# Kernel optimization log

Hardware: AMD Instinct MI355X
Metric: run time of the kernel (lower is better)

## Reference

```python
import jax, jax.numpy as jnp
import numpy as np

EPS = 1e-8  # torch F.cosine_similarity clamps norms at eps=1e-8


def setup_inputs() -> dict:
    key = jax.random.key(0)
    N, M, D = 1024, 20, 768  # speakers, utterances/speaker, embed dim
    embeddings = jax.random.normal(key, (N, M, D), dtype=jnp.float32)
    w = jnp.asarray(10.0, dtype=jnp.float32)  # init_w
    b = jnp.asarray(-5.0, dtype=jnp.float32)  # init_b
    return {"embeddings": embeddings, "w": w, "b": b}


def reference(embeddings, w, b):
    N, M, D = embeddings.shape
    centroids = embeddings.mean(axis=1)  # [N, D]
    # cosine similarity as one fused GEMM on normalized vectors
    e = embeddings / jnp.maximum(
        jnp.linalg.norm(embeddings, axis=-1, keepdims=True), EPS)
    c = centroids / jnp.maximum(
        jnp.linalg.norm(centroids, axis=-1, keepdims=True), EPS)
    # sim[j, i, m] = cos(e[i, m], centroid[j])  -- matches the torch loop/stack
    sim = jnp.einsum('imd,jd->jim', e, c)
    logits = w * sim + b  # [N_j, N_i, M]
    # torch: view(N*N, M).transpose(0,1).reshape(-1, N)
    #   => row index r = m*N + j, column i
    logits = jnp.transpose(logits, (2, 0, 1)).reshape(N * M, N)
    # torch labels: arange(N) expanded over M -> labels[r] = r // M
    labels = jnp.repeat(jnp.arange(N), M)
    logp = jax.nn.log_softmax(logits, axis=-1)
    loss = -jnp.mean(logp[jnp.arange(N * M), labels])
    return loss
```

## Files before the change

kernel.cpp:

```cpp
#include <hip/hip_runtime.h>
#include <hip/hip_bf16.h>
#include <cstdint>

#define N_SPK 1024
#define M_UTT 20
#define D_DIM 768
#define NM_ROWS (N_SPK * M_UTT)

static constexpr float EPS = 1e-8f;

#define WAIT_VM0   0x0F70
#define WAIT_LGKM0 0xC07F

typedef __attribute__((ext_vector_type(4))) float floatx4;

__device__ __forceinline__ void load16_to_lds(const void* g, void* l) {
    __builtin_amdgcn_global_load_lds(
        (const __attribute__((address_space(1))) uint32_t*)g,
        (__attribute__((address_space(3))) uint32_t*)l, 16, 0, 0);
}

__device__ __forceinline__ float wave_sum(float v) {
    #pragma unroll
    for (int o = 32; o > 0; o >>= 1) v += __shfl_xor(v, o);
    return v;
}

__device__ __forceinline__ unsigned short fp8pk(float a, float b) {
    return (unsigned short)(__builtin_amdgcn_cvt_pk_fp8_f32(a, b, 0, false) & 0xFFFF);
}

__global__ __launch_bounds__(384) void prep_kernel(const float* __restrict__ emb,
                                                   unsigned char* __restrict__ ehat,
                                                   unsigned char* __restrict__ chat,
                                                   int* __restrict__ ctr,
                                                   float* __restrict__ accum) {
    const int i = blockIdx.x;
    const int t = threadIdx.x;
    const int wave = t >> 6, lane = t & 63;

    if (i == 0 && t == 0) { *ctr = 0; *accum = 0.f; }

    const float2* src = (const float2*)(emb + (size_t)i * M_UTT * D_DIM);

    float2 v[M_UTT];
    float ss[M_UTT];
    float2 cen = {0.f, 0.f};
    #pragma unroll
    for (int m = 0; m < M_UTT; ++m) {
        const float2 x = src[m * 384 + t];
        v[m] = x;
        ss[m] = x.x * x.x + x.y * x.y;
        cen.x += x.x; cen.y += x.y;
    }
    cen.x *= (1.f / M_UTT); cen.y *= (1.f / M_UTT);
    float css = cen.x * cen.x + cen.y * cen.y;

    __shared__ float red[M_UTT + 1][6];
    #pragma unroll
    for (int m = 0; m < M_UTT; ++m) {
        const float s = wave_sum(ss[m]);
        if (lane == 0) red[m][wave] = s;
    }
    {
        const float s = wave_sum(css);
        if (lane == 0) red[M_UTT][wave] = s;
    }
    __syncthreads();

    #pragma unroll
    for (int m = 0; m < M_UTT; ++m) {
        const float tot = red[m][0] + red[m][1] + red[m][2] +
                          red[m][3] + red[m][4] + red[m][5];
        const float rn = 1.0f / fmaxf(sqrtf(tot), EPS);
        ((unsigned short*)(ehat + ((size_t)(m * N_SPK + i)) * D_DIM))[t] =
            fp8pk(v[m].x * rn, v[m].y * rn);
    }
    {
        const float tot = red[M_UTT][0] + red[M_UTT][1] + red[M_UTT][2] +
                          red[M_UTT][3] + red[M_UTT][4] + red[M_UTT][5];
        const float rn = 1.0f / fmaxf(sqrtf(tot), EPS);
        ((unsigned short*)(chat + (size_t)i * D_DIM))[t] =
            fp8pk(cen.x * rn, cen.y * rn);
    }
}

__global__ __launch_bounds__(64) void gemm_fused_kernel(
        const unsigned char* __restrict__ ehat,
        const unsigned char* __restrict__ chat,
        const float* __restrict__ wp,
        float* __restrict__ Psum,
        float* __restrict__ T) {
    __shared__ unsigned char As[64 * 128];
    __shared__ unsigned char Bs[64 * 128];

    const int lane = threadIdx.x;
    const int c = lane & 15;
    const int quad = lane >> 4;

    const int xcd = blockIdx.x & 7;
    const int idx = blockIdx.x >> 3;
    const int bu  = xcd * 40 + (idx >> 4);
    const int bj  = idx & 15;
    const int m   = bu >> 4;
    const int rb  = bu & 15;
    const int u0  = bu * 64;
    const int j0  = bj * 64;

    const unsigned char* Ag = ehat + (size_t)u0 * D_DIM;
    const unsigned char* Bg = chat + (size_t)j0 * D_DIM;

    int goff[8];
    #pragma unroll
    for (int s = 0; s < 8; ++s) {
        const int ci  = s * 64 + lane;
        const int row = ci >> 3;
        const int q   = (ci & 7) ^ (row & 7);
        goff[s] = row * D_DIM + q * 16;
    }

    int slotA[4][4], slotB[4][4];
    #pragma unroll
    for (int ks = 0; ks < 4; ++ks) {
        const int q = ks * 2 + (quad >> 1);
        #pragma unroll
        for (int f = 0; f < 4; ++f) {
            const int r = f * 16 + c;
            slotA[ks][f] = (r * 8 + (q ^ (r & 7))) * 16 + (quad & 1) * 8;
            slotB[ks][f] = slotA[ks][f];
        }
    }

    floatx4 acc[4][4] = {};

    #pragma unroll
    for (int s = 0; s < 8; ++s) {
        load16_to_lds(Ag + goff[s], As + (s * 64 + lane) * 16);
        load16_to_lds(Bg + goff[s], Bs + (s * 64 + lane) * 16);
    }

    for (int kt = 0; kt < 6; ++kt) {
        __builtin_amdgcn_s_waitcnt(WAIT_VM0);

        #pragma unroll
        for (int ks = 0; ks < 4; ++ks) {
            long af[4], bf[4];
            #pragma unroll
            for (int it = 0; it < 4; ++it)
                af[it] = *(const long*)(As + slotA[ks][it]);
            #pragma unroll
            for (int jt = 0; jt < 4; ++jt)
                bf[jt] = *(const long*)(Bs + slotB[ks][jt]);

            #pragma unroll
            for (int it = 0; it < 4; ++it)
                #pragma unroll
                for (int jt = 0; jt < 4; ++jt)
                    acc[it][jt] = __builtin_amdgcn_mfma_f32_16x16x32_fp8_fp8(
                        af[it], bf[jt], acc[it][jt], 0, 0, 0);
        }

        if (kt < 5) {
            const int k0 = (kt + 1) * 128;
            __builtin_amdgcn_s_waitcnt(WAIT_LGKM0);
            #pragma unroll
            for (int s = 0; s < 8; ++s) {
                load16_to_lds(Ag + goff[s] + k0, As + (s * 64 + lane) * 16);
                load16_to_lds(Bg + goff[s] + k0, Bs + (s * 64 + lane) * 16);
            }
        }
    }

    const float w = wp[0];

    #pragma unroll
    for (int jt = 0; jt < 4; ++jt) {
        float sm = 0.f;
        #pragma unroll
        for (int it = 0; it < 4; ++it)
            #pragma unroll
            for (int r = 0; r < 4; ++r)
                sm += __expf(w * (acc[it][jt][r] - 1.0f));
        sm += __shfl_xor(sm, 16);
        sm += __shfl_xor(sm, 32);
        if (quad == 0) Psum[(size_t)bu * N_SPK + j0 + jt * 16 + c] = sm;
    }

    #pragma unroll
    for (int it = 0; it < 4; ++it) {
        #pragma unroll
        for (int jt = 0; jt < 4; ++jt) {
            const int col = j0 + jt * 16 + c;
            const int g = m * N_SPK + col;
            const int istar = g / M_UTT;
            const int rloc = rb * 64 + it * 16 + quad * 4;
            #pragma unroll
            for (int r = 0; r < 4; ++r) {
                if (rloc + r == istar) T[g] = acc[it][jt][r];
            }
        }
    }
}

__global__ void combine_kernel(const float* __restrict__ Psum,
                               const float* __restrict__ T,
                               const float* __restrict__ wp,
                               int* __restrict__ ctr,
                               float* __restrict__ accum,
                               float* __restrict__ out) {
    const int p = blockIdx.x * 256 + threadIdx.x;
    const int m = p >> 10;
    const int j = p & 1023;
    const float w = wp[0];

    float S = 0.f;
    #pragma unroll
    for (int rb = 0; rb < 16; ++rb)
        S += Psum[(size_t)(m * 16 + rb) * N_SPK + j];
    const float term = w * (T[p] - 1.0f) - __logf(S);

    __shared__ float red[256];
    red[threadIdx.x] = term;
    __syncthreads();
    for (int o = 128; o > 0; o >>= 1) {
        if (threadIdx.x < o) red[threadIdx.x] += red[threadIdx.x + o];
        __syncthreads();
    }
    if (threadIdx.x == 0) {
        atomicAdd(accum, red[0]);
        __threadfence();
        const int old = atomicAdd(ctr, 1);
        if (old == 79) {
            const float a = atomicAdd(accum, 0.0f);
            out[0] = -a / (float)NM_ROWS;
        }
    }
}

extern "C" void kernel_launch(void* const* d_in, const int* in_sizes, int n_in,
                              void* d_out, int out_size, void* d_ws, size_t ws_size,
                              hipStream_t stream) {
    const float* emb = (const float*)d_in[0];
    const float* wp  = (const float*)d_in[1];
    float* out = (float*)d_out;

    char* ws = (char*)d_ws;
    unsigned char* ehat = (unsigned char*)(ws);
    unsigned char* chat = (unsigned char*)(ws + 15728640);
    float* Psum  = (float*)(ws + 16515072);
    float* T     = (float*)(ws + 17825792);
    int*   ctr   = (int*)  (ws + 17907712);
    float* accum = (float*)(ws + 17907716);

    prep_kernel<<<dim3(N_SPK), dim3(384), 0, stream>>>(emb, ehat, chat, ctr, accum);
    gemm_fused_kernel<<<dim3(5120), dim3(64), 0, stream>>>(ehat, chat, wp, Psum, T);
    combine_kernel<<<dim3(80), dim3(256), 0, stream>>>(Psum, T, wp, ctr, accum, out);
}
```

Before: 139.4 us.

## Use 128x128 four-wave GEMM tiles with double-buffered LDS K-slices

Replaces the single-wave 64x64 GEMM block with a 256-thread block computing a 128x128 tile, where each wave owns one 64x64 quadrant. Operand tiles loaded into LDS are shared across waves. The K loop now uses 64-byte slices with a double-buffered LDS ping-pong: the next slice is prefetched while the current one is consumed, and iterations are separated by __syncthreads. This is meant to cut global/L2 traffic through more tile reuse and to overlap loads with MFMA work, at the cost of block-wide barriers and lower block count (1280 blocks).

```diff
diff --git a/kernel.cpp b/kernel.cpp
--- a/kernel.cpp
+++ b/kernel.cpp
@@ -8,9 +8,6 @@
 #define NM_ROWS (N_SPK * M_UTT)
 
 static constexpr float EPS = 1e-8f;
-
-#define WAIT_VM0   0x0F70
-#define WAIT_LGKM0 0xC07F
 
 typedef __attribute__((ext_vector_type(4))) float floatx4;
 
@@ -85,72 +82,91 @@
     }
 }
 
-__global__ __launch_bounds__(64) void gemm_fused_kernel(
+__global__ __launch_bounds__(256, 5) void gemm_fused_kernel(
         const unsigned char* __restrict__ ehat,
         const unsigned char* __restrict__ chat,
         const float* __restrict__ wp,
         float* __restrict__ Psum,
         float* __restrict__ T) {
-    __shared__ unsigned char As[64 * 128];
-    __shared__ unsigned char Bs[64 * 128];
-
-    const int lane = threadIdx.x;
-    const int c = lane & 15;
+    __shared__ unsigned char As[2][128 * 64];
+    __shared__ unsigned char Bs[2][128 * 64];
+
+    const int t    = threadIdx.x;
+    const int lane = t & 63;
+    const int wid  = t >> 6;
+    const int c    = lane & 15;
     const int quad = lane >> 4;
+    const int wr   = wid >> 1;
+    const int wc   = wid & 1;
 
     const int xcd = blockIdx.x & 7;
     const int idx = blockIdx.x >> 3;
-    const int bu  = xcd * 40 + (idx >> 4);
-    const int bj  = idx & 15;
-    const int m   = bu >> 4;
-    const int rb  = bu & 15;
-    const int u0  = bu * 64;
-    const int j0  = bj * 64;
+    const int bu  = xcd * 20 + (idx >> 3);
+    const int bj  = idx & 7;
+    const int m   = bu >> 3;
+    const int rb8 = bu & 7;
+    const int u0  = bu * 128;
+    const int j0  = bj * 128;
 
     const unsigned char* Ag = ehat + (size_t)u0 * D_DIM;
     const unsigned char* Bg = chat + (size_t)j0 * D_DIM;
 
-    int goff[8];
-    #pragma unroll
-    for (int s = 0; s < 8; ++s) {
-        const int ci  = s * 64 + lane;
-        const int row = ci >> 3;
-        const int q   = (ci & 7) ^ (row & 7);
-        goff[s] = row * D_DIM + q * 16;
-    }
-
-    int slotA[4][4], slotB[4][4];
-    #pragma unroll
-    for (int ks = 0; ks < 4; ++ks) {
+    int goff[2];
+    #pragma unroll
+    for (int s = 0; s < 2; ++s) {
+        const int ci  = s * 256 + wid * 64 + lane;
+        const int row = ci >> 2;
+        const int qg  = (ci & 3) ^ ((row >> 1) & 3);
+        goff[s] = row * D_DIM + qg * 16;
+    }
+
+    int slotA[2][4], slotB[2][4];
+    #pragma unroll
+    for (int ks = 0; ks < 2; ++ks) {
         const int q = ks * 2 + (quad >> 1);
         #pragma unroll
         for (int f = 0; f < 4; ++f) {
-            const int r = f * 16 + c;
-            slotA[ks][f] = (r * 8 + (q ^ (r & 7))) * 16 + (quad & 1) * 8;
-            slotB[ks][f] = slotA[ks][f];
+            const int rA = wr * 64 + f * 16 + c;
+            const int rB = wc * 64 + f * 16 + c;
+            slotA[ks][f] = rA * 64 + ((q ^ ((rA >> 1) & 3)) * 16) + (quad & 1) * 8;
+            slotB[ks][f] = rB * 64 + ((q ^ ((rB >> 1) & 3)) * 16) + (quad & 1) * 8;
         }
     }
 
     floatx4 acc[4][4] = {};
 
     #pragma unroll
-    for (int s = 0; s < 8; ++s) {
-        load16_to_lds(Ag + goff[s], As + (s * 64 + lane) * 16);
-        load16_to_lds(Bg + goff[s], Bs + (s * 64 + lane) * 16);
-    }
-
-    for (int kt = 0; kt < 6; ++kt) {
-        __builtin_amdgcn_s_waitcnt(WAIT_VM0);
-
-        #pragma unroll
-        for (int ks = 0; ks < 4; ++ks) {
+    for (int s = 0; s < 2; ++s) {
+        load16_to_lds(Ag + goff[s], &As[0][(s * 256 + wid * 64 + lane) * 16]);
+        load16_to_lds(Bg + goff[s], &Bs[0][(s * 256 + wid * 64 + lane) * 16]);
+    }
+    __syncthreads();
+
+    #pragma unroll
+    for (int kt = 0; kt < 12; ++kt) {
+        const int cur = kt & 1;
+        const int nxt = cur ^ 1;
+
+        if (kt < 11) {
+            const int k0 = (kt + 1) * 64;
+            #pragma unroll
+            for (int s = 0; s < 2; ++s) {
+                load16_to_lds(Ag + goff[s] + k0,
+                              &As[nxt][(s * 256 + wid * 64 + lane) * 16]);
+                load16_to_lds(Bg + goff[s] + k0,
+                              &Bs[nxt][(s * 256 + wid * 64 + lane) * 16]);
+            }
+        }
+
+        #pragma unroll
+        for (int ks = 0; ks < 2; ++ks) {
             long af[4], bf[4];
             #pragma unroll
-            for (int it = 0; it < 4; ++it)
-                af[it] = *(const long*)(As + slotA[ks][it]);
-            #pragma unroll
-            for (int jt = 0; jt < 4; ++jt)
-                bf[jt] = *(const long*)(Bs + slotB[ks][jt]);
+            for (int f = 0; f < 4; ++f)
+                af[f] = *(const long*)(&As[cur][slotA[ks][f]]);
+            #pragma unroll
+            for (int f = 0; f < 4; ++f)
+                bf[f] = *(const long*)(&Bs[cur][slotB[ks][f]]);
 
             #pragma unroll
             for (int it = 0; it < 4; ++it)
@@ -160,18 +176,11 @@
                         af[it], bf[jt], acc[it][jt], 0, 0, 0);
         }
 
-        if (kt < 5) {
-            const int k0 = (kt + 1) * 128;
-            __builtin_amdgcn_s_waitcnt(WAIT_LGKM0);
-            #pragma unroll
-            for (int s = 0; s < 8; ++s) {
-                load16_to_lds(Ag + goff[s] + k0, As + (s * 64 + lane) * 16);
-                load16_to_lds(Bg + goff[s] + k0, Bs + (s * 64 + lane) * 16);
-            }
-        }
+        if (kt < 11) __syncthreads();
     }
 
     const float w = wp[0];
+    const int rb320 = bu * 2 + wr;
 
     #pragma unroll
     for (int jt = 0; jt < 4; ++jt) {
@@ -183,17 +192,18 @@
                 sm += __expf(w * (acc[it][jt][r] - 1.0f));
         sm += __shfl_xor(sm, 16);
         sm += __shfl_xor(sm, 32);
-        if (quad == 0) Psum[(size_t)bu * N_SPK + j0 + jt * 16 + c] = sm;
+        if (quad == 0)
+            Psum[(size_t)rb320 * N_SPK + j0 + wc * 64 + jt * 16 + c] = sm;
     }
 
     #pragma unroll
     for (int it = 0; it < 4; ++it) {
         #pragma unroll
         for (int jt = 0; jt < 4; ++jt) {
-            const int col = j0 + jt * 16 + c;
+            const int col = j0 + wc * 64 + jt * 16 + c;
             const int g = m * N_SPK + col;
             const int istar = g / M_UTT;
-            const int rloc = rb * 64 + it * 16 + quad * 4;
+            const int rloc = rb8 * 128 + wr * 64 + it * 16 + quad * 4;
             #pragma unroll
             for (int r = 0; r < 4; ++r) {
                 if (rloc + r == istar) T[g] = acc[it][jt][r];
@@ -253,6 +263,6 @@
     float* accum = (float*)(ws + 17907716);
 
     prep_kernel<<<dim3(N_SPK), dim3(384), 0, stream>>>(emb, ehat, chat, ctr, accum);
-    gemm_fused_kernel<<<dim3(5120), dim3(64), 0, stream>>>(ehat, chat, wp, Psum, T);
+    gemm_fused_kernel<<<dim3(1280), dim3(256), 0, stream>>>(ehat, chat, wp, Psum, T);
     combine_kernel<<<dim3(80), dim3(256), 0, stream>>>(Psum, T, wp, ctr, accum, out);
 }
```

After: 157.8 us. +13.2%, slower.
